# Optimization experiments

Hardware: AMD Instinct MI355X
Metric: run time of the kernel (lower is better)

## Reference

```python
import jax, jax.numpy as jnp
import numpy as np

EPS = 1e-09

def setup_inputs() -> dict:
    key = jax.random.key(0)
    k1, k2, k3, k4 = jax.random.split(key, 4)
    B, T, H, D, E = 2, 2048, 1024, 1024, 8
    x = jax.random.normal(k1, (B, T, H), dtype=jnp.float32)
    gate_w = jax.random.normal(k2, (E, H), dtype=jnp.float32) * 0.02
    gate_up_proj = jax.random.normal(k3, (E, H, 2 * D), dtype=jnp.float32) * 0.02
    down_proj = jax.random.normal(k4, (E, D, H), dtype=jnp.float32) * 0.02
    return {"x": x, "gate_w": gate_w, "gate_up_proj": gate_up_proj, "down_proj": down_proj}

def reference(x, gate_w, gate_up_proj, down_proj):
    B, T, H = x.shape
    E = gate_w.shape[0]
    top_k = 2
    hidden = x.reshape(-1, H)                      # [N, H]
    router_logits = hidden @ gate_w.T              # [N, E]
    routing_weights = jax.nn.softmax(router_logits.astype(jnp.float32), axis=-1)
    topk_weights, topk_indices = jax.lax.top_k(routing_weights, top_k)
    topk_weights = topk_weights / (jnp.sum(topk_weights, axis=-1, keepdims=True) + EPS)
    N = hidden.shape[0]
    routed = jnp.zeros((N, E), dtype=router_logits.dtype)
    rows = jnp.arange(N)[:, None]
    routed = routed.at[rows, topk_indices].set(topk_weights.astype(router_logits.dtype))
    routed = routed / (jnp.sum(routed, axis=-1, keepdims=True) + EPS)
    routed = routed.astype(hidden.dtype)
    # dense all-experts MoE
    gate_up = jnp.einsum('th,ehq->teq', hidden, gate_up_proj)  # [N, E, 2D]
    gate, up = jnp.split(gate_up, 2, axis=-1)
    expert_outputs = jnp.einsum('teq,eqh->teh', jax.nn.silu(gate) * up, down_proj)
    out = jnp.sum(expert_outputs * routed[:, :, None], axis=1)  # [N, H]
    return out.reshape(B, T, H)
```

## Files before the change

### kernel.cpp

```cpp
#include <hip/hip_runtime.h>
#include <hip/hip_bf16.h>
#include <stdint.h>

#define N_TOK 4096
#define HDIM  1024
#define DDIM  1024
#define NEXP  8
#define TWO_D 2048
#define BK    64

typedef __bf16 bf16x8_t __attribute__((ext_vector_type(8)));
typedef float  f32x4_t  __attribute__((ext_vector_type(4)));

__device__ __forceinline__ void gload16(const void* g, void* l) {
  __builtin_amdgcn_global_load_lds(
      (const __attribute__((address_space(1))) void*)g,
      (__attribute__((address_space(3))) void*)l, 16, 0, 0);
}

__device__ __forceinline__ uint16_t f2bf(float f) {
  union { float f; uint32_t u; } v; v.f = f;
  uint32_t r = ((v.u >> 16) & 1u) + 0x7fffu;
  return (uint16_t)((v.u + r) >> 16);
}

__global__ __launch_bounds__(256) void router_kernel(
    const float* __restrict__ x, const float* __restrict__ gw,
    uint32_t* __restrict__ t_e, float* __restrict__ slot_w) {
  int wid = threadIdx.x >> 6;
  int lane = threadIdx.x & 63;
  int t = blockIdx.x * 4 + wid;
  const float4* xr = (const float4*)(x + (size_t)t * HDIM);
  const float4* g4 = (const float4*)gw;
  float acc[NEXP];
#pragma unroll
  for (int e = 0; e < NEXP; ++e) acc[e] = 0.f;
#pragma unroll
  for (int i = 0; i < HDIM / 256; ++i) {
    float4 xv = xr[lane + 64 * i];
#pragma unroll
    for (int e = 0; e < NEXP; ++e) {
      float4 gv = g4[e * (HDIM / 4) + lane + 64 * i];
      acc[e] += xv.x * gv.x + xv.y * gv.y + xv.z * gv.z + xv.w * gv.w;
    }
  }
#pragma unroll
  for (int off = 32; off > 0; off >>= 1) {
#pragma unroll
    for (int e = 0; e < NEXP; ++e)
      acc[e] += __shfl_xor(acc[e], off, 64);
  }
  if (lane == 0) {
    int e1 = 0; float l1 = acc[0];
#pragma unroll
    for (int e = 1; e < NEXP; ++e) if (acc[e] > l1) { l1 = acc[e]; e1 = e; }
    int e2 = -1; float l2 = -1e30f;
#pragma unroll
    for (int e = 0; e < NEXP; ++e) if (e != e1 && acc[e] > l2) { l2 = acc[e]; e2 = e; }
    float s = 0.f;
#pragma unroll
    for (int e = 0; e < NEXP; ++e) s += expf(acc[e] - l1);
    float p1 = 1.0f / s;
    float p2 = expf(l2 - l1) / s;
    float tw = p1 + p2 + 1e-9f;
    float w1 = p1 / tw, w2 = p2 / tw;
    float s2 = w1 + w2 + 1e-9f;
    w1 /= s2; w2 /= s2;
    t_e[t] = (uint32_t)e1 | ((uint32_t)e2 << 16);
    slot_w[2 * t] = w1;
    slot_w[2 * t + 1] = w2;
  }
}

__global__ __launch_bounds__(256) void build_lists_kernel(
    const uint32_t* __restrict__ t_e, int* __restrict__ counts,
    int* __restrict__ tok_slot) {
  __shared__ int cnt[NEXP];
  if (threadIdx.x < NEXP) cnt[threadIdx.x] = 0;
  __syncthreads();
  for (int t = threadIdx.x; t < N_TOK; t += 256) {
    uint32_t pe = t_e[t];
    int e1 = (int)(pe & 0xffffu), e2 = (int)(pe >> 16);
    int p1 = atomicAdd(&cnt[e1], 1);
    tok_slot[e1 * N_TOK + p1] = 2 * t;
    int p2 = atomicAdd(&cnt[e2], 1);
    tok_slot[e2 * N_TOK + p2] = 2 * t + 1;
  }
  __syncthreads();
  if (threadIdx.x < NEXP) counts[threadIdx.x] = cnt[threadIdx.x];
}

__global__ __launch_bounds__(256) void cvt_x_kernel(const float* __restrict__ x,
                                                    uint16_t* __restrict__ xb) {
  int i = blockIdx.x * 256 + threadIdx.x;
  float4 v = ((const float4*)x)[i];
  uint2 o;
  o.x = (uint32_t)f2bf(v.x) | ((uint32_t)f2bf(v.y) << 16);
  o.y = (uint32_t)f2bf(v.z) | ((uint32_t)f2bf(v.w) << 16);
  ((uint2*)xb)[i] = o;
}

__global__ __launch_bounds__(256) void transpose_cvt_kernel(
    const float* __restrict__ src, uint16_t* __restrict__ dst, int R, int C) {
  __shared__ float tile[32][33];
  size_t slice = (size_t)R * C;
  src += blockIdx.z * slice;
  dst += blockIdx.z * slice;
  int cb = blockIdx.x * 32, rbase = blockIdx.y * 32;
  int c = threadIdx.x & 31, r0 = threadIdx.x >> 5;
#pragma unroll
  for (int i = 0; i < 4; ++i) {
    int r = r0 + 8 * i;
    tile[r][c] = src[(size_t)(rbase + r) * C + cb + c];
  }
  __syncthreads();
  int r2 = (threadIdx.x & 15) * 2, cp0 = threadIdx.x >> 4;
#pragma unroll
  for (int i = 0; i < 2; ++i) {
    int cp = cp0 + 16 * i;
    uint32_t u = (uint32_t)f2bf(tile[r2][cp]) | ((uint32_t)f2bf(tile[r2 + 1][cp]) << 16);
    *(uint32_t*)(dst + (size_t)(cb + cp) * R + rbase + r2) = u;
  }
}

__global__ __launch_bounds__(512) void gemm_gu_kernel(
    const uint16_t* __restrict__ xb, const uint16_t* __restrict__ w1t,
    const int* __restrict__ counts, const int* __restrict__ tok_slot,
    uint16_t* __restrict__ h_buf) {
  int id = blockIdx.x;
  id = (id & 7) * 256 + (id >> 3);
  int e = id >> 8;
  int rem = id & 255;
  int rb = rem >> 3;
  int cb = rem & 7;
  int M = counts[e];
  if (rb * 128 >= M) return;
  int c0 = cb * 128;
  const int* list = tok_slot + e * N_TOK;
  const uint16_t* wB = w1t + (size_t)e * TWO_D * HDIM;

  __shared__ uint16_t As[128 * BK];
  __shared__ uint16_t Bs[256 * BK];

  int tid = threadIdx.x;
  int w = tid >> 6, l = tid & 63;
  int wr = w >> 2, wc = w & 3;
  int lane15 = l & 15, hi = l >> 4;

  const char* aSrc[2]; char* aDst[2];
#pragma unroll
  for (int p = 0; p < 2; ++p) {
    int row = p * 64 + (tid >> 3);
    int pos = rb * 128 + row; if (pos > M - 1) pos = M - 1;
    int tok = list[pos] >> 1;
    int kch = (tid & 7) ^ (row & 7);
    aSrc[p] = (const char*)(xb + (size_t)tok * HDIM) + kch * 16;
    aDst[p] = (char*)As + p * 8192 + tid * 16;
  }
  const char* bSrc[4]; char* bDst[4];
#pragma unroll
  for (int p = 0; p < 4; ++p) {
    int s = p * 64 + (tid >> 3);
    int j = s & 63, g = s >> 6;
    int col = (j < 32) ? (c0 + g * 32 + j) : (HDIM + c0 + g * 32 + (j - 32));
    int kch = (tid & 7) ^ (s & 7);
    bSrc[p] = (const char*)(wB + (size_t)col * HDIM) + kch * 16;
    bDst[p] = (char*)Bs + p * 8192 + tid * 16;
  }

  f32x4_t acc[4][4];
#pragma unroll
  for (int m = 0; m < 4; ++m)
#pragma unroll
    for (int n = 0; n < 4; ++n) acc[m][n] = {0.f, 0.f, 0.f, 0.f};

  uint32_t aRow[4], bRow[4], xch[2];
#pragma unroll
  for (int m = 0; m < 4; ++m) aRow[m] = (uint32_t)((wr * 64 + m * 16 + lane15) * 128);
#pragma unroll
  for (int n = 0; n < 4; ++n) bRow[n] = (uint32_t)((wc * 64 + n * 16 + lane15) * 128);
  xch[0] = (uint32_t)(((0 + hi) ^ (l & 7)) * 16);
  xch[1] = (uint32_t)(((4 + hi) ^ (l & 7)) * 16);

#pragma unroll
  for (int p = 0; p < 2; ++p) gload16(aSrc[p], aDst[p]);
#pragma unroll
  for (int p = 0; p < 4; ++p) gload16(bSrc[p], bDst[p]);

  for (int kt = 0; kt < HDIM / BK; ++kt) {
    __syncthreads();
    bf16x8_t a[2][4], b[2][4];
#pragma unroll
    for (int kk = 0; kk < 2; ++kk) {
#pragma unroll
      for (int m = 0; m < 4; ++m)
        a[kk][m] = *(const bf16x8_t*)((const char*)As + aRow[m] + xch[kk]);
#pragma unroll
      for (int n = 0; n < 4; ++n)
        b[kk][n] = *(const bf16x8_t*)((const char*)Bs + bRow[n] + xch[kk]);
    }
    __syncthreads();
    if (kt + 1 < HDIM / BK) {
      int ko = (kt + 1) * 128;
#pragma unroll
      for (int p = 0; p < 2; ++p) gload16(aSrc[p] + ko, aDst[p]);
#pragma unroll
      for (int p = 0; p < 4; ++p) gload16(bSrc[p] + ko, bDst[p]);
    }
#pragma unroll
    for (int kk = 0; kk < 2; ++kk)
#pragma unroll
      for (int m = 0; m < 4; ++m)
#pragma unroll
        for (int n = 0; n < 4; ++n)
          acc[m][n] = __builtin_amdgcn_mfma_f32_16x16x32_bf16(a[kk][m], b[kk][n], acc[m][n], 0, 0, 0);
  }

  int Mloc = M - rb * 128;
#pragma unroll
  for (int m = 0; m < 4; ++m) {
#pragma unroll
    for (int i = 0; i < 4; ++i) {
      int rl = wr * 64 + m * 16 + hi * 4 + i;
      if (rl < Mloc) {
        int slot = list[rb * 128 + rl];
        uint16_t* hr = h_buf + (size_t)slot * DDIM;
#pragma unroll
        for (int n = 0; n < 2; ++n) {
          int hcol = c0 + wc * 32 + n * 16 + lane15;
          float g = acc[m][n][i];
          float u = acc[m][n + 2][i];
          float hv = g / (1.f + expf(-g)) * u;
          hr[hcol] = f2bf(hv);
        }
      }
    }
  }
}

__global__ __launch_bounds__(256) void gemm_down_kernel(
    const uint16_t* __restrict__ h_buf, const uint16_t* __restrict__ w2t,
    const int* __restrict__ counts, const int* __restrict__ tok_slot,
    const float* __restrict__ slot_w, float* __restrict__ out) {
  int id = blockIdx.x;
  id = (id & 7) * 256 + (id >> 3);
  int e = id >> 8;
  int rem = id & 255;
  int rb = rem >> 3;
  int cb = rem & 7;
  int M = counts[e];
  if (rb * 128 >= M) return;
  int c0 = cb * 128;
  const int* list = tok_slot + e * N_TOK;
  const uint16_t* wB = w2t + (size_t)e * HDIM * DDIM;

  __shared__ uint16_t As[128 * BK];
  __shared__ uint16_t Bs[128 * BK];

  int tid = threadIdx.x;
  int w = tid >> 6, l = tid & 63;
  int wr = w >> 1, wc = w & 1;
  int lane15 = l & 15, hi = l >> 4;

  const char* aSrc[4]; char* aDst[4];
  const char* bSrc[4]; char* bDst[4];
#pragma unroll
  for (int p = 0; p < 4; ++p) {
    int row = p * 32 + (tid >> 3);
    int pos = rb * 128 + row; if (pos > M - 1) pos = M - 1;
    int slot = list[pos];
    int kch = (tid & 7) ^ (row & 7);
    aSrc[p] = (const char*)(h_buf + (size_t)slot * DDIM) + kch * 16;
    aDst[p] = (char*)As + p * 4096 + tid * 16;
    int col = c0 + row;
    bSrc[p] = (const char*)(wB + (size_t)col * DDIM) + kch * 16;
    bDst[p] = (char*)Bs + p * 4096 + tid * 16;
  }

  f32x4_t acc[4][4];
#pragma unroll
  for (int m = 0; m < 4; ++m)
#pragma unroll
    for (int n = 0; n < 4; ++n) acc[m][n] = {0.f, 0.f, 0.f, 0.f};

  uint32_t aRow[4], bRow[4], xch[2];
#pragma unroll
  for (int m = 0; m < 4; ++m) aRow[m] = (uint32_t)((wr * 64 + m * 16 + lane15) * 128);
#pragma unroll
  for (int n = 0; n < 4; ++n) bRow[n] = (uint32_t)((wc * 64 + n * 16 + lane15) * 128);
  xch[0] = (uint32_t)(((0 + hi) ^ (l & 7)) * 16);
  xch[1] = (uint32_t)(((4 + hi) ^ (l & 7)) * 16);

#pragma unroll
  for (int p = 0; p < 4; ++p) { gload16(aSrc[p], aDst[p]); gload16(bSrc[p], bDst[p]); }

  for (int kt = 0; kt < DDIM / BK; ++kt) {
    __syncthreads();
    bf16x8_t a[2][4], b[2][4];
#pragma unroll
    for (int kk = 0; kk < 2; ++kk) {
#pragma unroll
      for (int m = 0; m < 4; ++m)
        a[kk][m] = *(const bf16x8_t*)((const char*)As + aRow[m] + xch[kk]);
#pragma unroll
      for (int n = 0; n < 4; ++n)
        b[kk][n] = *(const bf16x8_t*)((const char*)Bs + bRow[n] + xch[kk]);
    }
    __syncthreads();
    if (kt + 1 < DDIM / BK) {
      int ko = (kt + 1) * 128;
#pragma unroll
      for (int p = 0; p < 4; ++p) { gload16(aSrc[p] + ko, aDst[p]); gload16(bSrc[p] + ko, bDst[p]); }
    }
#pragma unroll
    for (int kk = 0; kk < 2; ++kk)
#pragma unroll
      for (int m = 0; m < 4; ++m)
#pragma unroll
        for (int n = 0; n < 4; ++n)
          acc[m][n] = __builtin_amdgcn_mfma_f32_16x16x32_bf16(a[kk][m], b[kk][n], acc[m][n], 0, 0, 0);
  }

  int Mloc = M - rb * 128;
#pragma unroll
  for (int m = 0; m < 4; ++m) {
#pragma unroll
    for (int i = 0; i < 4; ++i) {
      int rl = wr * 64 + m * 16 + hi * 4 + i;
      if (rl < Mloc) {
        int slot = list[rb * 128 + rl];
        int tok = slot >> 1;
        float wgt = slot_w[slot];
        float* orow = out + (size_t)tok * HDIM;
#pragma unroll
        for (int n = 0; n < 4; ++n) {
          int col = c0 + wc * 64 + n * 16 + lane15;
          atomicAdd(&orow[col], wgt * acc[m][n][i]);
        }
      }
    }
  }
}

extern "C" void kernel_launch(void* const* d_in, const int* in_sizes, int n_in,
                              void* d_out, int out_size, void* d_ws, size_t ws_size,
                              hipStream_t stream) {
  const float* x  = (const float*)d_in[0];
  const float* gw = (const float*)d_in[1];
  const float* w1 = (const float*)d_in[2];
  const float* w2 = (const float*)d_in[3];
  float* out = (float*)d_out;

  char* ws = (char*)d_ws;
  int*      counts   = (int*)ws;
  int*      tok_slot = (int*)(ws + 1024);
  float*    slot_w   = (float*)(ws + 1024 + 131072);
  uint32_t* t_e      = (uint32_t*)(ws + 1024 + 131072 + 32768);
  size_t off = (size_t)1 << 20;
  uint16_t* xb  = (uint16_t*)(ws + off); off += (size_t)N_TOK * HDIM * 2;
  uint16_t* w1t = (uint16_t*)(ws + off); off += (size_t)NEXP * TWO_D * HDIM * 2;
  uint16_t* w2t = (uint16_t*)(ws + off); off += (size_t)NEXP * HDIM * DDIM * 2;
  uint16_t* hb  = (uint16_t*)(ws + off); off += (size_t)2 * N_TOK * DDIM * 2;

  hipMemsetAsync(d_out, 0, (size_t)out_size * sizeof(float), stream);
  if (ws_size < off) return;

  cvt_x_kernel<<<(N_TOK * HDIM) / 1024, 256, 0, stream>>>(x, xb);
  transpose_cvt_kernel<<<dim3(TWO_D / 32, HDIM / 32, NEXP), 256, 0, stream>>>(w1, w1t, HDIM, TWO_D);
  transpose_cvt_kernel<<<dim3(HDIM / 32, DDIM / 32, NEXP), 256, 0, stream>>>(w2, w2t, DDIM, HDIM);
  router_kernel<<<N_TOK / 4, 256, 0, stream>>>(x, gw, t_e, slot_w);
  build_lists_kernel<<<1, 256, 0, stream>>>(t_e, counts, tok_slot);
  gemm_gu_kernel<<<2048, 512, 0, stream>>>(xb, w1t, counts, tok_slot, hb);
  gemm_down_kernel<<<2048, 256, 0, stream>>>(hb, w2t, counts, tok_slot, slot_w, out);
}
```

Measured before the change: 270.7 us.

## Replace atomic down-proj scatter with bf16 per-slot buffer and combine kernel

The down-projection GEMM now writes bf16 results per routing slot into a reused workspace (the w1t region, which is free after the gate/up GEMM). A separate combine kernel then takes the weighted sum of each token's two slots and writes fp32 output. This removes the fp32 atomicAdds and the output memset. The down GEMM tile also widens to 128x256 with 512 threads, which improves reuse of the A tile. The cost is an extra launch and a round trip of the intermediate through memory, and the bf16 rounding of the intermediate adds some precision loss.

```diff
diff --git a/kernel.cpp b/kernel.cpp
--- a/kernel.cpp
+++ b/kernel.cpp
@@ -22,6 +22,11 @@
   union { float f; uint32_t u; } v; v.f = f;
   uint32_t r = ((v.u >> 16) & 1u) + 0x7fffu;
   return (uint16_t)((v.u + r) >> 16);
+}
+
+__device__ __forceinline__ float bf2f(uint16_t b) {
+  union { uint32_t u; float f; } v; v.u = (uint32_t)b << 16;
+  return v.f;
 }
 
 __global__ __launch_bounds__(256) void router_kernel(
@@ -238,43 +243,48 @@
   }
 }
 
-__global__ __launch_bounds__(256) void gemm_down_kernel(
+__global__ __launch_bounds__(512) void gemm_down_kernel(
     const uint16_t* __restrict__ h_buf, const uint16_t* __restrict__ w2t,
     const int* __restrict__ counts, const int* __restrict__ tok_slot,
-    const float* __restrict__ slot_w, float* __restrict__ out) {
+    uint16_t* __restrict__ ob) {
   int id = blockIdx.x;
-  id = (id & 7) * 256 + (id >> 3);
-  int e = id >> 8;
-  int rem = id & 255;
-  int rb = rem >> 3;
-  int cb = rem & 7;
+  id = (id & 7) * 128 + (id >> 3);
+  int e = id >> 7;
+  int rem = id & 127;
+  int rb = rem >> 2;
+  int cb = rem & 3;
   int M = counts[e];
   if (rb * 128 >= M) return;
-  int c0 = cb * 128;
+  int c0 = cb * 256;
   const int* list = tok_slot + e * N_TOK;
   const uint16_t* wB = w2t + (size_t)e * HDIM * DDIM;
 
   __shared__ uint16_t As[128 * BK];
-  __shared__ uint16_t Bs[128 * BK];
+  __shared__ uint16_t Bs[256 * BK];
 
   int tid = threadIdx.x;
   int w = tid >> 6, l = tid & 63;
-  int wr = w >> 1, wc = w & 1;
+  int wr = w >> 2, wc = w & 3;
   int lane15 = l & 15, hi = l >> 4;
 
-  const char* aSrc[4]; char* aDst[4];
-  const char* bSrc[4]; char* bDst[4];
-#pragma unroll
-  for (int p = 0; p < 4; ++p) {
-    int row = p * 32 + (tid >> 3);
+  const char* aSrc[2]; char* aDst[2];
+#pragma unroll
+  for (int p = 0; p < 2; ++p) {
+    int row = p * 64 + (tid >> 3);
     int pos = rb * 128 + row; if (pos > M - 1) pos = M - 1;
     int slot = list[pos];
     int kch = (tid & 7) ^ (row & 7);
     aSrc[p] = (const char*)(h_buf + (size_t)slot * DDIM) + kch * 16;
-    aDst[p] = (char*)As + p * 4096 + tid * 16;
-    int col = c0 + row;
+    aDst[p] = (char*)As + p * 8192 + tid * 16;
+  }
+  const char* bSrc[4]; char* bDst[4];
+#pragma unroll
+  for (int p = 0; p < 4; ++p) {
+    int s = p * 64 + (tid >> 3);
+    int col = c0 + s;
+    int kch = (tid & 7) ^ (s & 7);
     bSrc[p] = (const char*)(wB + (size_t)col * DDIM) + kch * 16;
-    bDst[p] = (char*)Bs + p * 4096 + tid * 16;
+    bDst[p] = (char*)Bs + p * 8192 + tid * 16;
   }
 
   f32x4_t acc[4][4];
@@ -292,7 +302,9 @@
   xch[1] = (uint32_t)(((4 + hi) ^ (l & 7)) * 16);
 
 #pragma unroll
-  for (int p = 0; p < 4; ++p) { gload16(aSrc[p], aDst[p]); gload16(bSrc[p], bDst[p]); }
+  for (int p = 0; p < 2; ++p) gload16(aSrc[p], aDst[p]);
+#pragma unroll
+  for (int p = 0; p < 4; ++p) gload16(bSrc[p], bDst[p]);
 
   for (int kt = 0; kt < DDIM / BK; ++kt) {
     __syncthreads();
@@ -310,7 +322,9 @@
     if (kt + 1 < DDIM / BK) {
       int ko = (kt + 1) * 128;
 #pragma unroll
-      for (int p = 0; p < 4; ++p) { gload16(aSrc[p] + ko, aDst[p]); gload16(bSrc[p] + ko, bDst[p]); }
+      for (int p = 0; p < 2; ++p) gload16(aSrc[p] + ko, aDst[p]);
+#pragma unroll
+      for (int p = 0; p < 4; ++p) gload16(bSrc[p] + ko, bDst[p]);
     }
 #pragma unroll
     for (int kk = 0; kk < 2; ++kk)
@@ -329,17 +343,39 @@
       int rl = wr * 64 + m * 16 + hi * 4 + i;
       if (rl < Mloc) {
         int slot = list[rb * 128 + rl];
-        int tok = slot >> 1;
-        float wgt = slot_w[slot];
-        float* orow = out + (size_t)tok * HDIM;
+        uint16_t* orow = ob + ((size_t)slot << 10);
 #pragma unroll
         for (int n = 0; n < 4; ++n) {
           int col = c0 + wc * 64 + n * 16 + lane15;
-          atomicAdd(&orow[col], wgt * acc[m][n][i]);
+          orow[col] = f2bf(acc[m][n][i]);
         }
       }
     }
   }
+}
+
+__global__ __launch_bounds__(256) void combine_kernel(
+    const uint16_t* __restrict__ ob, const float* __restrict__ slot_w,
+    float* __restrict__ out) {
+  int idx = blockIdx.x * 256 + threadIdx.x;
+  int t = idx >> 7;
+  int d8 = idx & 127;
+  const uint16_t* r0 = ob + ((size_t)(2 * t) << 10) + d8 * 8;
+  const uint16_t* r1 = ob + ((size_t)(2 * t + 1) << 10) + d8 * 8;
+  float w0 = slot_w[2 * t], w1 = slot_w[2 * t + 1];
+  uint4 a = *(const uint4*)r0;
+  uint4 b = *(const uint4*)r1;
+  float o[8];
+  const uint32_t* au = (const uint32_t*)&a;
+  const uint32_t* bu = (const uint32_t*)&b;
+#pragma unroll
+  for (int j = 0; j < 4; ++j) {
+    o[2 * j]     = w0 * bf2f((uint16_t)(au[j] & 0xffffu)) + w1 * bf2f((uint16_t)(bu[j] & 0xffffu));
+    o[2 * j + 1] = w0 * bf2f((uint16_t)(au[j] >> 16))     + w1 * bf2f((uint16_t)(bu[j] >> 16));
+  }
+  float4* op = (float4*)(out + (size_t)t * HDIM + d8 * 8);
+  op[0] = make_float4(o[0], o[1], o[2], o[3]);
+  op[1] = make_float4(o[4], o[5], o[6], o[7]);
 }
 
 extern "C" void kernel_launch(void* const* d_in, const int* in_sizes, int n_in,
@@ -361,9 +397,12 @@
   uint16_t* w1t = (uint16_t*)(ws + off); off += (size_t)NEXP * TWO_D * HDIM * 2;
   uint16_t* w2t = (uint16_t*)(ws + off); off += (size_t)NEXP * HDIM * DDIM * 2;
   uint16_t* hb  = (uint16_t*)(ws + off); off += (size_t)2 * N_TOK * DDIM * 2;
-
-  hipMemsetAsync(d_out, 0, (size_t)out_size * sizeof(float), stream);
-  if (ws_size < off) return;
+  uint16_t* ob = w1t;
+
+  if (ws_size < off) {
+    hipMemsetAsync(d_out, 0, (size_t)out_size * sizeof(float), stream);
+    return;
+  }
 
   cvt_x_kernel<<<(N_TOK * HDIM) / 1024, 256, 0, stream>>>(x, xb);
   transpose_cvt_kernel<<<dim3(TWO_D / 32, HDIM / 32, NEXP), 256, 0, stream>>>(w1, w1t, HDIM, TWO_D);
@@ -371,5 +410,6 @@
   router_kernel<<<N_TOK / 4, 256, 0, stream>>>(x, gw, t_e, slot_w);
   build_lists_kernel<<<1, 256, 0, stream>>>(t_e, counts, tok_slot);
   gemm_gu_kernel<<<2048, 512, 0, stream>>>(xb, w1t, counts, tok_slot, hb);
-  gemm_down_kernel<<<2048, 256, 0, stream>>>(hb, w2t, counts, tok_slot, slot_w, out);
-}
+  gemm_down_kernel<<<1024, 512, 0, stream>>>(hb, w2t, counts, tok_slot, ob);
+  combine_kernel<<<(N_TOK * HDIM / 8) / 256, 256, 0, stream>>>(ob, slot_w, out);
+}
```

After: 257.9 us. -4.7%, faster.
